# Kernel optimization log

Measured on AMD Instinct MI355X. Metric: run time of the kernel, lower is better.

Reference implementation:

```python
import jax, jax.numpy as jnp
import numpy as np

N_NODES = 20000
N_EDGES = 640000
HID = 256
IN_F, IN_SIZE = 6, 6
OUT_F, FH = 6, 3
EDGE_DIM = 8
T_DIM, S_DIM = 4, 6
N_LAYERS = 5


def setup_inputs() -> dict:
    key = jax.random.key(0)
    ks = jax.random.split(key, 32)
    g = lambda i, shape, scale=0.05: jax.random.normal(ks[i], shape, dtype=jnp.float32) * scale
    inp = {
        "x": jax.random.normal(ks[0], (N_NODES, IN_F, IN_SIZE), dtype=jnp.float32),
        "edge_index": jax.random.randint(ks[1], (2, N_EDGES), 0, N_NODES, dtype=jnp.int32),
        "edge_attr": jax.random.normal(ks[2], (N_EDGES, EDGE_DIM), dtype=jnp.float32),
        "t": jax.random.normal(ks[3], (N_NODES, T_DIM), dtype=jnp.float32),
        "s": jax.random.normal(ks[4], (N_NODES, S_DIM), dtype=jnp.float32),
        # embedder
        "W_emb": g(5, (IN_F * IN_SIZE, HID)), "b_emb": jnp.zeros((HID,), jnp.float32),
        # spatio-temporal encoder: t/s linear embeds + fusion over concat(x, te, se)
        "W_t": g(6, (T_DIM, HID)), "b_t": jnp.zeros((HID,), jnp.float32),
        "W_s": g(7, (S_DIM, HID)), "b_s": jnp.zeros((HID,), jnp.float32),
        "W_f": g(8, (3 * HID, HID)), "b_f": jnp.zeros((HID,), jnp.float32),
        # layernorm
        "ln_g": jnp.ones((HID,), jnp.float32), "ln_b": jnp.zeros((HID,), jnp.float32),
        # 5 TransformerConv layers (heads=1): query/key/value/edge/skip linears
        "Wq": g(9, (N_LAYERS, HID, HID)), "bq": jnp.zeros((N_LAYERS, HID), jnp.float32),
        "Wk": g(10, (N_LAYERS, HID, HID)), "bk": jnp.zeros((N_LAYERS, HID), jnp.float32),
        "Wv": g(11, (N_LAYERS, HID, HID)), "bv": jnp.zeros((N_LAYERS, HID), jnp.float32),
        "We": g(12, (N_LAYERS, EDGE_DIM, HID)), "be": jnp.zeros((N_LAYERS, HID), jnp.float32),
        "Wskip": g(13, (N_LAYERS, HID, HID)), "bskip": jnp.zeros((N_LAYERS, HID), jnp.float32),
        # decoder
        "W_dec": g(14, (HID, OUT_F * FH)), "b_dec": jnp.zeros((OUT_F * FH,), jnp.float32),
    }
    return inp


def _layernorm(x, g, b, eps=1e-5):
    mu = jnp.mean(x, axis=-1, keepdims=True)
    var = jnp.mean((x - mu) ** 2, axis=-1, keepdims=True)
    return (x - mu) * jax.lax.rsqrt(var + eps) * g + b


def _transformer_conv(x, src, dst, edge_attr, Wq, bq, Wk, bk, Wv, bv, We, be, Wskip, bskip):
    n = x.shape[0]
    d = x.shape[1]
    q = x @ Wq + bq                      # [n, d]
    k = x @ Wk + bk
    v = x @ Wv + bv
    e = edge_attr @ We + be              # [E, d]
    kj = k[src] + e                      # gather + edge fuse [E, d]
    vj = v[src] + e
    alpha = jnp.sum(q[dst] * kj, axis=-1) / jnp.sqrt(jnp.float32(d))  # [E]
    # segment softmax over incoming edges of each destination node
    m = jax.ops.segment_max(alpha, dst, num_segments=n)
    a = jnp.exp(alpha - m[dst])
    denom = jax.ops.segment_sum(a, dst, num_segments=n)
    w = a / (denom[dst] + 1e-16)
    out = jax.ops.segment_sum(vj * w[:, None], dst, num_segments=n)  # [n, d]
    return out + x @ Wskip + bskip       # root/skip connection


def reference(x, edge_index, edge_attr, t, s,
              W_emb, b_emb, W_t, b_t, W_s, b_s, W_f, b_f, ln_g, ln_b,
              Wq, bq, Wk, bk, Wv, bv, We, be, Wskip, bskip, W_dec, b_dec):
    n = x.shape[0]
    h = x.reshape(n, -1) @ W_emb + b_emb
    te = t @ W_t + b_t
    se = s @ W_s + b_s
    h = jnp.concatenate([h, te, se], axis=-1) @ W_f + b_f   # spatio-temporal fuse
    h = jax.nn.relu(_layernorm(h, ln_g, ln_b))
    src, dst = edge_index[0], edge_index[1]
    for i in range(N_LAYERS):
        h = jax.nn.relu(_transformer_conv(h, src, dst, edge_attr,
                                          Wq[i], bq[i], Wk[i], bk[i], Wv[i], bv[i],
                                          We[i], be[i], Wskip[i], bskip[i]))
    out = h @ W_dec + b_dec
    return out.reshape(n, OUT_F, FH)
```

## Files before the change

kernel.cpp:

```cpp
#include <hip/hip_runtime.h>
#include <hip/hip_fp8.h>
#include <math.h>

#define NN 20000
#define NPAD 20096
#define NE 640000
#define NOUT 1152
#define GSS 272
#define KVB 512
#define CAP 80
#define RECB 32
#define SCQ 0.09016994f
#define ISCL 8.8057e-5f
#define TIDX(r,k) ((((r)>>4)*4096) + (((k)>>3)*128) + (((r)&15)*8) + ((k)&7))

typedef _Float16 f16;
typedef f16 f16x8 __attribute__((ext_vector_type(8)));
typedef f16 f16x4 __attribute__((ext_vector_type(4)));
typedef f16 h2    __attribute__((ext_vector_type(2)));
typedef float f32x4 __attribute__((ext_vector_type(4)));
typedef float f32x2 __attribute__((ext_vector_type(2)));

static __device__ __forceinline__ float fdot2(h2 a, h2 b, float c) {
#if __has_builtin(__builtin_amdgcn_fdot2)
  return __builtin_amdgcn_fdot2(a, b, c, false);
#else
  return c + (float)a[0]*(float)b[0] + (float)a[1]*(float)b[1];
#endif
}

static __device__ __forceinline__ float fast_exp2(float x) {
#if __has_builtin(__builtin_amdgcn_exp2f)
  return __builtin_amdgcn_exp2f(x);
#else
  return exp2f(x);
#endif
}

static __device__ __forceinline__ int sdot4(unsigned a, unsigned b, int c) {
#if __has_builtin(__builtin_amdgcn_sdot4)
  return __builtin_amdgcn_sdot4((int)a, (int)b, c, false);
#else
  int r = c;
  #pragma unroll
  for (int i = 0; i < 4; i++) {
    int ai = ((int)((a >> (8*i)) & 255) ^ 128) - 128;
    int bi = ((int)((b >> (8*i)) & 255) ^ 128) - 128;
    r += ai*bi;
  }
  return r;
#endif
}

static __device__ __forceinline__ unsigned pack_i8x4(float a, float b, float c, float d) {
  int i0 = (int)rintf(a), i1 = (int)rintf(b), i2 = (int)rintf(c), i3 = (int)rintf(d);
  i0 = max(-127, min(127, i0)); i1 = max(-127, min(127, i1));
  i2 = max(-127, min(127, i2)); i3 = max(-127, min(127, i3));
  return (unsigned)(i0 & 255) | ((unsigned)(i1 & 255) << 8)
       | ((unsigned)(i2 & 255) << 16) | ((unsigned)(i3 & 255) << 24);
}

static __device__ __forceinline__ unsigned pack_fp8x4(float a, float b, float c, float d) {
#if __has_builtin(__builtin_amdgcn_cvt_pk_fp8_f32)
  int r = __builtin_amdgcn_cvt_pk_fp8_f32(a, b, 0, false);
  r = __builtin_amdgcn_cvt_pk_fp8_f32(c, d, r, true);
  return (unsigned)r;
#else
  __hip_fp8_e4m3 w(a), x2(b), y(c), z(d);
  return (unsigned)w.__x | ((unsigned)x2.__x<<8) | ((unsigned)y.__x<<16) | ((unsigned)z.__x<<24);
#endif
}

template<bool HI>
static __device__ __forceinline__ f32x2 unpack_fp8x2(unsigned v) {
#if __has_builtin(__builtin_amdgcn_cvt_pk_f32_fp8)
  return __builtin_amdgcn_cvt_pk_f32_fp8((int)v, HI);
#else
  unsigned s = HI ? (v >> 16) : (v & 0xffff);
  __hip_fp8_e4m3 a, b; a.__x = (unsigned char)(s & 0xff); b.__x = (unsigned char)(s >> 8);
  return (f32x2){ (float)a, (float)b };
#endif
}

__global__ __launch_bounds__(256) void k_prep_all(
    const float* __restrict__ W_emb, const float* __restrict__ W_t,
    const float* __restrict__ W_s,   const float* __restrict__ W_f,
    const float* __restrict__ b_emb, const float* __restrict__ b_t,
    const float* __restrict__ b_s,   const float* __restrict__ b_f,
    const float* __restrict__ Wq, const float* __restrict__ Wk,
    const float* __restrict__ Wv, const float* __restrict__ Wsk,
    const float* __restrict__ We, const float* __restrict__ be,
    const float* __restrict__ bq, const float* __restrict__ bk,
    const float* __restrict__ bv, const float* __restrict__ bsk,
    f16* __restrict__ Wch, float* __restrict__ bc,
    f16* __restrict__ WT, float* __restrict__ b_all,
    f16* __restrict__ hA, f16* __restrict__ hB)
{
  __shared__ float smem[64*65];
  int b = blockIdx.x;
  int tid = threadIdx.x;

  if (b < 47) {
    int r = b, c = tid;
    if (r < 36) {
      float a = 0.f;
      for (int m = 0; m < 256; m++) a += W_emb[r*256+m] * W_f[m*256+c];
      Wch[r*256+c] = (f16)a;
    } else if (r < 40) {
      int rr = r - 36; float a = 0.f;
      for (int m = 0; m < 256; m++) a += W_t[rr*256+m] * W_f[(256+m)*256+c];
      Wch[r*256+c] = (f16)a;
    } else if (r < 46) {
      int rr = r - 40; float a = 0.f;
      for (int m = 0; m < 256; m++) a += W_s[rr*256+m] * W_f[(512+m)*256+c];
      Wch[r*256+c] = (f16)a;
    } else {
      float a = b_f[c];
      for (int m = 0; m < 256; m++) a += b_emb[m]*W_f[m*256+c];
      for (int m = 0; m < 256; m++) a += b_t[m]*W_f[(256+m)*256+c];
      for (int m = 0; m < 256; m++) a += b_s[m]*W_f[(512+m)*256+c];
      bc[c] = a;
    }
  } else if (b < 367) {
    float (*lds)[65] = (float(*)[65])smem;
    int bb = b - 47;
    int nt = bb & 3, kt = (bb >> 2) & 3, mat = (bb >> 4) & 3, L = bb >> 6;
    const float* src = (mat == 0 ? Wq : mat == 1 ? Wk : mat == 2 ? Wv : Wsk) + (size_t)L*65536;
    int k0 = kt*64, n0 = nt*64;
    int c = tid & 63, r4 = tid >> 6;
    #pragma unroll
    for (int rr = 0; rr < 16; rr++) {
      int row = rr*4 + r4;
      lds[row][c] = src[(size_t)(k0 + row)*256 + n0 + c];
    }
    __syncthreads();
    f16* dst = WT + (size_t)L*294912;
    int nl = tid & 63, kb2 = tid >> 6;
    int ng = mat*256 + n0 + nl;
    #pragma unroll
    for (int half = 0; half < 2; half++) {
      int kb = kb2 + half*4;
      f16x8 v;
      #pragma unroll
      for (int e = 0; e < 8; e++) v[e] = (f16)lds[kb*8 + e][nl];
      *(f16x8*)(dst + TIDX(ng, k0 + kb*8)) = v;
    }
  } else if (b < 412) {
    float* vec = smem;
    int bb = b - 367;
    int L = bb / 9;
    int t = bb % 9;
    vec[tid] = (t < 8) ? We[(size_t)L*2048 + t*256 + tid] : be[(size_t)L*256 + tid];
    __syncthreads();
    int wave = tid >> 6, lane = tid & 63;
    for (int k = wave; k < 256; k += 4) {
      f32x4 wq = *(const f32x4*)(Wq + (size_t)L*65536 + (size_t)k*256 + lane*4);
      f32x4 vv = *(const f32x4*)(vec + lane*4);
      float d = wq[0]*vv[0] + wq[1]*vv[1] + wq[2]*vv[2] + wq[3]*vv[3];
      #pragma unroll
      for (int o = 32; o; o >>= 1) d += __shfl_xor(d, o, 64);
      if (lane == 0) WT[(size_t)L*294912 + TIDX(1024 + t, k)] = (f16)d;
    }
  } else if (b < 417) {
    int L = b - 412;
    for (int c = tid; c < NOUT; c += 256) {
      float v;
      if (c < 256)       v = bq [L*256+c];
      else if (c < 512)  v = bk [L*256+(c-256)];
      else if (c < 768)  v = bv [L*256+(c-512)];
      else if (c < 1024) v = bsk[L*256+(c-768)];
      else if (c < 1032) {
        int t = c-1024; float a = 0.f;
        for (int m = 0; m < 256; m++) a += bq[L*256+m]*We[(size_t)L*2048 + t*256 + m];
        v = a;
      } else if (c == 1032) {
        float a = 0.f;
        for (int m = 0; m < 256; m++) a += bq[L*256+m]*be[L*256+m];
        v = a;
      } else v = 0.f;
      b_all[(size_t)L*NOUT + c] = v;
    }
  } else {
    f16* p = (b == 417 ? hA : hB) + (size_t)NN*256;
    f16x8 z = {};
    for (int i = tid; i < (NPAD-NN)*256/8; i += 256)
      *(f16x8*)(p + (size_t)i*8) = z;
  }
}

__global__ void k_scatter(const int* __restrict__ ei, const float* __restrict__ eattr,
                          int* cnt, char* __restrict__ rec)
{
  int e = blockIdx.x*256 + threadIdx.x;
  if (e < NE) {
    int d = ei[NE + e];
    int pos = atomicAdd(&cnt[d], 1);
    char* rp = rec + (size_t)(d*CAP + pos)*RECB;
    f32x4 a0 = *(const f32x4*)(eattr + (size_t)e*8);
    f32x4 a1 = *(const f32x4*)(eattr + (size_t)e*8 + 4);
    f16x8 ea = { (f16)a0[0],(f16)a0[1],(f16)a0[2],(f16)a0[3],
                 (f16)a1[0],(f16)a1[1],(f16)a1[2],(f16)a1[3] };
    *(f16x8*)rp = ea;
    *(int*)(rp + 16) = ei[e];
  }
}

__global__ __launch_bounds__(256) void k_encoder(
    const float* __restrict__ x, const float* __restrict__ t, const float* __restrict__ s,
    const f16* __restrict__ Wch, const float* __restrict__ bc,
    const float* __restrict__ lng, const float* __restrict__ lnb,
    f16* __restrict__ h)
{
  __shared__ f16 Wcs[46*256];
  __shared__ float xin[16][48];
  __shared__ float bcs[256], lgs[256], lbs[256];
  int tid = threadIdx.x;
  int u0 = blockIdx.x * 16;
  for (int i = tid; i < 46*128; i += 256)
    ((unsigned int*)Wcs)[i] = ((const unsigned int*)Wch)[i];
  bcs[tid] = bc[tid]; lgs[tid] = lng[tid]; lbs[tid] = lnb[tid];
  for (int i = tid; i < 576; i += 256) xin[i/36][i%36] = x[(size_t)u0*36 + i];
  if (tid < 64) xin[tid>>2][36 + (tid&3)] = t[(size_t)u0*4 + tid];
  if (tid < 96) xin[tid/6][40 + tid%6] = s[(size_t)u0*6 + tid];
  __syncthreads();
  int node = tid >> 4, cg = tid & 15;
  int u = u0 + node;
  float acc[16];
  #pragma unroll
  for (int j = 0; j < 16; j++) acc[j] = bcs[cg*16+j];
  for (int r = 0; r < 46; r++) {
    float xv = xin[node][r];
    const h2* wr = (const h2*)(Wcs + r*256 + cg*16);
    #pragma unroll
    for (int j2 = 0; j2 < 8; j2++) {
      h2 w2 = wr[j2];
      acc[j2*2]   += xv * (float)w2[0];
      acc[j2*2+1] += xv * (float)w2[1];
    }
  }
  float sm = 0.f, sq = 0.f;
  #pragma unroll
  for (int j = 0; j < 16; j++) { sm += acc[j]; sq += acc[j]*acc[j]; }
  #pragma unroll
  for (int o = 1; o < 16; o <<= 1) { sm += __shfl_xor(sm, o, 64); sq += __shfl_xor(sq, o, 64); }
  float mu  = sm * (1.f/256.f);
  float var = sq * (1.f/256.f) - mu*mu;
  float rin = rsqrtf(var + 1e-5f);
  f16x8 o0, o1;
  #pragma unroll
  for (int j = 0; j < 8; j++) {
    int c = cg*16 + j;
    float v = (acc[j]-mu)*rin*lgs[c] + lbs[c];
    o0[j] = (f16)fmaxf(v, 0.f);
  }
  #pragma unroll
  for (int j = 0; j < 8; j++) {
    int c = cg*16 + 8 + j;
    float v = (acc[8+j]-mu)*rin*lgs[c] + lbs[c];
    o1[j] = (f16)fmaxf(v, 0.f);
  }
  *(f16x8*)(h + TIDX(u, cg*16))   = o0;
  *(f16x8*)(h + TIDX(u, cg*16+8)) = o1;
}

__global__ __launch_bounds__(256) void k_gemm(
    const f16* __restrict__ A, const f16* __restrict__ BT,
    const float* __restrict__ bias,
    unsigned char* __restrict__ qt8, unsigned char* __restrict__ kvt,
    f16* __restrict__ gsk)
{
  const int NWG = (NPAD/128)*9;
  const int Q = NWG >> 3, R = NWG & 7;
  int bid = blockIdx.x;
  int xcd = bid & 7, jj = bid >> 3;
  int wg = (xcd < R ? xcd*(Q+1) : R*(Q+1) + (xcd-R)*Q) + jj;
  int bmt = wg / 9, bnt = wg - bmt*9;

  int tid = threadIdx.x;
  int wave = tid >> 6, lane = tid & 63;
  int wm = wave >> 1, wn = wave & 1;
  int bm = bmt*128 + wm*64;
  int bn = bnt*128 + wn*64;
  int lr = lane & 15;
  int kg = lane >> 4;
  f32x4 acc[4][4];
  #pragma unroll
  for (int i = 0; i < 4; i++)
    #pragma unroll
    for (int j = 0; j < 4; j++) acc[i][j] = (f32x4){0.f,0.f,0.f,0.f};

  const f16* Ab = A  + (size_t)(bm >> 4)*4096 + kg*128 + lr*8;
  const f16* Bb = BT + (size_t)(bn >> 4)*4096 + kg*128 + lr*8;
  #pragma unroll
  for (int k0 = 0; k0 < 256; k0 += 32) {
    f16x8 af[4], bf[4];
    #pragma unroll
    for (int i = 0; i < 4; i++) af[i] = *(const f16x8*)(Ab + i*4096 + k0*16);
    #pragma unroll
    for (int j = 0; j < 4; j++) bf[j] = *(const f16x8*)(Bb + j*4096 + k0*16);
    #pragma unroll
    for (int i = 0; i < 4; i++)
      #pragma unroll
      for (int j = 0; j < 4; j++)
        acc[i][j] = __builtin_amdgcn_mfma_f32_16x16x32_f16(bf[j], af[i], acc[i][j], 0, 0, 0);
  }

  #pragma unroll
  for (int j = 0; j < 4; j++) {
    int cb0 = bn + j*16;
    if (cb0 >= 1040) continue;
    int colq = cb0 + kg*4;
    f32x4 bv = *(const f32x4*)(bias + colq);
    #pragma unroll
    for (int i = 0; i < 4; i++) {
      int row = bm + i*16 + lr;
      float v0 = acc[i][j][0]+bv[0], v1 = acc[i][j][1]+bv[1];
      float v2 = acc[i][j][2]+bv[2], v3 = acc[i][j][3]+bv[3];
      if (cb0 < 256) {
        *(unsigned*)(qt8 + (size_t)row*256 + colq) = pack_i8x4(v0*32.f, v1*32.f, v2*32.f, v3*32.f);
      } else if (cb0 < 512) {
        *(unsigned*)(kvt + (size_t)row*KVB + (colq-256)) = pack_i8x4(v0*32.f, v1*32.f, v2*32.f, v3*32.f);
      } else if (cb0 < 768) {
        *(unsigned*)(kvt + (size_t)row*KVB + 256 + (colq-512)) = pack_fp8x4(v0, v1, v2, v3);
      } else if (cb0 < 1024) {
        f16x4 st = { (f16)v0, (f16)v1, (f16)v2, (f16)v3 };
        *(f16x4*)(gsk + (size_t)row*GSS + (colq-768)) = st;
      } else {
        f16x4 st = { (f16)(v0*SCQ), (f16)(v1*SCQ), (f16)(v2*SCQ), (f16)(v3*SCQ) };
        *(f16x4*)(gsk + (size_t)row*GSS + 256 + (colq-1024)) = st;
      }
    }
  }
}

__global__ __launch_bounds__(256) void k_alpha(
    const unsigned char* __restrict__ qt8, const unsigned char* __restrict__ kvt,
    const f16* __restrict__ gsk, char* __restrict__ rec,
    const int* __restrict__ cnt, float* __restrict__ stats)
{
  int wid = threadIdx.x >> 6, lane = threadIdx.x & 63;
  int u = __builtin_amdgcn_readfirstlane(blockIdx.x*4 + wid);
  int deg = cnt[u];
  const uint4* qp = (const uint4*)(qt8 + (size_t)u*256);
  uint4 q[16];
  #pragma unroll
  for (int c = 0; c < 16; c++) q[c] = qp[c];
  const f16* gb = gsk + (size_t)u*GSS;
  f16x8 qe8 = *(const f16x8*)(gb + 256);
  float qbv = (float)gb[264];
  size_t ub = (size_t)u*CAP;

  float ssum = 0.f;
  float ae[8];
  #pragma unroll
  for (int j = 0; j < 8; j++) ae[j] = 0.f;

  for (int i = lane; i < deg; i += 64) {
    char* rp = rec + (ub + i)*RECB;
    f16x8 ea = *(const f16x8*)rp;
    int sn = *(const int*)(rp + 16);
    const uint4* kp = (const uint4*)(kvt + (size_t)sn*KVB);
    int di = 0;
    #pragma unroll
    for (int c = 0; c < 16; c++) {
      uint4 kw = kp[c];
      di = sdot4(kw.x, q[c].x, di);
      di = sdot4(kw.y, q[c].y, di);
      di = sdot4(kw.z, q[c].z, di);
      di = sdot4(kw.w, q[c].w, di);
    }
    float edot = 0.f;
    edot = fdot2((h2){ea[0],ea[1]}, (h2){qe8[0],qe8[1]}, edot);
    edot = fdot2((h2){ea[2],ea[3]}, (h2){qe8[2],qe8[3]}, edot);
    edot = fdot2((h2){ea[4],ea[5]}, (h2){qe8[4],qe8[5]}, edot);
    edot = fdot2((h2){ea[6],ea[7]}, (h2){qe8[6],qe8[7]}, edot);
    float w = fast_exp2((float)di*ISCL + edot + qbv);
    *(float*)(rp + 20) = w;
    ssum += w;
    #pragma unroll
    for (int j = 0; j < 8; j++) ae[j] += w*(float)ea[j];
  }

  #pragma unroll
  for (int o = 1; o < 64; o <<= 1) {
    ssum += __shfl_xor(ssum, o, 64);
    #pragma unroll
    for (int j = 0; j < 8; j++) ae[j] += __shfl_xor(ae[j], o, 64);
  }
  if (lane == 0) {
    float* sp = stats + (size_t)u*12;
    sp[0] = ssum;
    *(f32x4*)(sp + 4) = (f32x4){ae[0], ae[1], ae[2], ae[3]};
    *(f32x4*)(sp + 8) = (f32x4){ae[4], ae[5], ae[6], ae[7]};
  }
}

__global__ __launch_bounds__(256) void k_attn2(
    const unsigned char* __restrict__ kvt, const f16* __restrict__ gsk,
    const char* __restrict__ rec,
    const float* __restrict__ WeL, const float* __restrict__ beL,
    const int* __restrict__ cnt, const float* __restrict__ stats,
    f16* __restrict__ hout)
{
  int wid  = threadIdx.x >> 6;
  int lane = threadIdx.x & 63;
  int grp  = lane >> 4;
  int gl   = lane & 15;
  int u = blockIdx.x*4 + wid;
  int deg = cnt[u];
  size_t ub = (size_t)u*CAP;

  float av[16];
  #pragma unroll
  for (int j = 0; j < 16; j++) av[j] = 0.f;

  #pragma unroll 2
  for (int i = grp; i < deg; i += 4) {
    const char* rp = rec + (ub + i)*RECB;
    int2 sw = *(const int2*)(rp + 16);
    float w = __int_as_float(sw.y);
    uint4 vw = *(const uint4*)(kvt + (size_t)sw.x*KVB + 256 + gl*16);
    f32x2 p;
    p = unpack_fp8x2<false>(vw.x); av[0]  += w*p[0]; av[1]  += w*p[1];
    p = unpack_fp8x2<true >(vw.x); av[2]  += w*p[0]; av[3]  += w*p[1];
    p = unpack_fp8x2<false>(vw.y); av[4]  += w*p[0]; av[5]  += w*p[1];
    p = unpack_fp8x2<true >(vw.y); av[6]  += w*p[0]; av[7]  += w*p[1];
    p = unpack_fp8x2<false>(vw.z); av[8]  += w*p[0]; av[9]  += w*p[1];
    p = unpack_fp8x2<true >(vw.z); av[10] += w*p[0]; av[11] += w*p[1];
    p = unpack_fp8x2<false>(vw.w); av[12] += w*p[0]; av[13] += w*p[1];
    p = unpack_fp8x2<true >(vw.w); av[14] += w*p[0]; av[15] += w*p[1];
  }

  #pragma unroll
  for (int j = 0; j < 16; j++) {
    av[j] += __shfl_xor(av[j], 16, 64);
    av[j] += __shfl_xor(av[j], 32, 64);
  }

  const float* sp = stats + (size_t)u*12;
  float ssum = sp[0];
  f32x4 aeA = *(const f32x4*)(sp + 4);
  f32x4 aeB = *(const f32x4*)(sp + 8);
  float inv = 1.f/(ssum + 1e-16f);

  int cb = gl*16 + grp*4;
  f16x4 sk = *(const f16x4*)(gsk + (size_t)u*GSS + cb);
  f16 res[4];
  #pragma unroll
  for (int t = 0; t < 4; t++) {
    int c = cb + t;
    float o = av[grp*4+t];
    o += aeA[0]*WeL[0*256+c] + aeA[1]*WeL[1*256+c] + aeA[2]*WeL[2*256+c] + aeA[3]*WeL[3*256+c];
    o += aeB[0]*WeL[4*256+c] + aeB[1]*WeL[5*256+c] + aeB[2]*WeL[6*256+c] + aeB[3]*WeL[7*256+c];
    o += ssum*beL[c];
    o = o*inv + (float)sk[t];
    res[t] = (f16)fmaxf(o, 0.f);
  }
  f16x4 outp = { res[0], res[1], res[2], res[3] };
  *(f16x4*)(hout + TIDX(u, cb)) = outp;
}

__global__ __launch_bounds__(256) void k_decoder(
    const f16* __restrict__ h, const float* __restrict__ Wd,
    const float* __restrict__ bd, float* __restrict__ out)
{
  int n0 = blockIdx.x*32;
  __shared__ float hs[32*256];
  int tid = threadIdx.x;
  for (int j = tid; j < 32*32; j += 256) {
    int node = j >> 5, c8 = (j & 31)*8;
    f16x8 v = *(const f16x8*)(h + TIDX(n0 + node, c8));
    float* dst = &hs[node*256 + c8];
    #pragma unroll
    for (int e = 0; e < 8; e++) dst[e] = (float)v[e];
  }
  __syncthreads();
  for (int o = tid; o < 32*18; o += 256) {
    int ln = o/18, col = o - ln*18;
    int node = n0 + ln;
    float acc = bd[col];
    const float* hr = &hs[ln*256];
    #pragma unroll 4
    for (int k4 = 0; k4 < 64; k4++) {
      f32x4 hv = *(const f32x4*)(hr + k4*4);
      acc += hv[0]*Wd[(k4*4+0)*18+col] + hv[1]*Wd[(k4*4+1)*18+col]
           + hv[2]*Wd[(k4*4+2)*18+col] + hv[3]*Wd[(k4*4+3)*18+col];
    }
    out[(size_t)node*18 + col] = acc;
  }
}

extern "C" void kernel_launch(void* const* d_in, const int* in_sizes, int n_in,
                              void* d_out, int out_size, void* d_ws, size_t ws_size,
                              hipStream_t stream)
{
  const float* x     = (const float*)d_in[0];
  const int*   ei    = (const int*)  d_in[1];
  const float* eattr = (const float*)d_in[2];
  const float* t     = (const float*)d_in[3];
  const float* s     = (const float*)d_in[4];
  const float* W_emb = (const float*)d_in[5];
  const float* b_emb = (const float*)d_in[6];
  const float* W_t   = (const float*)d_in[7];
  const float* b_t   = (const float*)d_in[8];
  const float* W_s   = (const float*)d_in[9];
  const float* b_s   = (const float*)d_in[10];
  const float* W_f   = (const float*)d_in[11];
  const float* b_f   = (const float*)d_in[12];
  const float* ln_g  = (const float*)d_in[13];
  const float* ln_b  = (const float*)d_in[14];
  const float* Wq    = (const float*)d_in[15];
  const float* bq    = (const float*)d_in[16];
  const float* Wk    = (const float*)d_in[17];
  const float* bk    = (const float*)d_in[18];
  const float* Wv    = (const float*)d_in[19];
  const float* bv    = (const float*)d_in[20];
  const float* We    = (const float*)d_in[21];
  const float* be    = (const float*)d_in[22];
  const float* Wsk   = (const float*)d_in[23];
  const float* bsk   = (const float*)d_in[24];
  const float* W_dec = (const float*)d_in[25];
  const float* b_dec = (const float*)d_in[26];

  float* wsf = (float*)d_ws;
  size_t off = 0;
  float* bc    = wsf + off; off += 256;
  float* b_all = wsf + off; off += (size_t)5*NOUT;
  f16*   Wch   = (f16*)(wsf + off); off += (size_t)46*256/2;
  f16*   WT    = (f16*)(wsf + off); off += (size_t)5*294912/2;
  unsigned char* qt8 = (unsigned char*)(wsf + off); off += (size_t)NPAD*256/4;
  unsigned char* kvt = (unsigned char*)(wsf + off); off += (size_t)NPAD*KVB/4;
  f16*   gsk   = (f16*)(wsf + off); off += (size_t)NPAD*GSS/2;
  f16*   hA    = (f16*)(wsf + off); off += (size_t)NPAD*256/2;
  f16*   hB    = (f16*)(wsf + off); off += (size_t)NPAD*256/2;
  char*  rec   = (char*)(wsf + off); off += (size_t)NN*CAP*RECB/4;
  float* stats = wsf + off; off += (size_t)NN*12;
  int*   cnt   = (int*)(wsf + off); off += NN;

  (void)hipMemsetAsync(cnt, 0, NN*sizeof(int), stream);
  k_prep_all<<<419, 256, 0, stream>>>(W_emb, W_t, W_s, W_f, b_emb, b_t, b_s, b_f,
                                      Wq, Wk, Wv, Wsk, We, be, bq, bk, bv, bsk,
                                      Wch, bc, WT, b_all, hA, hB);
  k_scatter <<<(NE+255)/256, 256, 0, stream>>>(ei, eattr, cnt, rec);

  k_encoder <<<NN/16, 256, 0, stream>>>(x, t, s, Wch, bc, ln_g, ln_b, hA);

  f16* hin = hA;
  f16* hot = hB;
  for (int L = 0; L < 5; L++) {
    k_gemm<<<(NPAD/128)*9, 256, 0, stream>>>(hin, WT + (size_t)L*294912,
                                             b_all + (size_t)L*NOUT, qt8, kvt, gsk);
    k_alpha<<<NN/4, 256, 0, stream>>>(qt8, kvt, gsk, rec, cnt, stats);
    k_attn2<<<NN/4, 256, 0, stream>>>(kvt, gsk, rec, We + (size_t)L*2048,
                                      be + (size_t)L*256, cnt, stats, hot);
    f16* tmp = hin; hin = hot; hot = tmp;
  }
  k_decoder<<<NN/32, 256, 0, stream>>>(hin, W_dec, b_dec, (float*)d_out);
}
```

Baseline: 602.6 us.

## Fuse alpha and aggregation kernels via LDS and double-buffer GEMM operand loads

Merges the score kernel and the weighted-aggregation kernel into one per-destination-node kernel. Per-edge source/weight pairs now go to shared memory instead of being written back into the edge records, and the softmax stats stay in registers instead of a global stats buffer. This removes one launch per layer plus the global write and re-read of weights and stats. Separately, the GEMM main loop is hand-unrolled with two register sets so the next K-slice loads overlap the current MFMAs, at the cost of more registers. There is no barrier between the LDS writes and reads, which relies on each wave touching only its own slot.

```diff
diff --git a/kernel.cpp b/kernel.cpp
--- a/kernel.cpp
+++ b/kernel.cpp
@@ -291,19 +291,75 @@
 
   const f16* Ab = A  + (size_t)(bm >> 4)*4096 + kg*128 + lr*8;
   const f16* Bb = BT + (size_t)(bn >> 4)*4096 + kg*128 + lr*8;
-  #pragma unroll
-  for (int k0 = 0; k0 < 256; k0 += 32) {
-    f16x8 af[4], bf[4];
-    #pragma unroll
-    for (int i = 0; i < 4; i++) af[i] = *(const f16x8*)(Ab + i*4096 + k0*16);
-    #pragma unroll
-    for (int j = 0; j < 4; j++) bf[j] = *(const f16x8*)(Bb + j*4096 + k0*16);
-    #pragma unroll
-    for (int i = 0; i < 4; i++)
-      #pragma unroll
-      for (int j = 0; j < 4; j++)
-        acc[i][j] = __builtin_amdgcn_mfma_f32_16x16x32_f16(bf[j], af[i], acc[i][j], 0, 0, 0);
-  }
+
+  f16x8 a0,a1,a2,a3,b0,b1,b2,b3;
+  f16x8 c0,c1,c2,c3,d0,d1,d2,d3;
+
+#define LDX(K0) \
+  a0 = *(const f16x8*)(Ab + 0*4096 + (K0)*16); a1 = *(const f16x8*)(Ab + 1*4096 + (K0)*16); \
+  a2 = *(const f16x8*)(Ab + 2*4096 + (K0)*16); a3 = *(const f16x8*)(Ab + 3*4096 + (K0)*16); \
+  b0 = *(const f16x8*)(Bb + 0*4096 + (K0)*16); b1 = *(const f16x8*)(Bb + 1*4096 + (K0)*16); \
+  b2 = *(const f16x8*)(Bb + 2*4096 + (K0)*16); b3 = *(const f16x8*)(Bb + 3*4096 + (K0)*16);
+#define LDY(K0) \
+  c0 = *(const f16x8*)(Ab + 0*4096 + (K0)*16); c1 = *(const f16x8*)(Ab + 1*4096 + (K0)*16); \
+  c2 = *(const f16x8*)(Ab + 2*4096 + (K0)*16); c3 = *(const f16x8*)(Ab + 3*4096 + (K0)*16); \
+  d0 = *(const f16x8*)(Bb + 0*4096 + (K0)*16); d1 = *(const f16x8*)(Bb + 1*4096 + (K0)*16); \
+  d2 = *(const f16x8*)(Bb + 2*4096 + (K0)*16); d3 = *(const f16x8*)(Bb + 3*4096 + (K0)*16);
+#define MMX() \
+  acc[0][0]=__builtin_amdgcn_mfma_f32_16x16x32_f16(b0,a0,acc[0][0],0,0,0); \
+  acc[0][1]=__builtin_amdgcn_mfma_f32_16x16x32_f16(b1,a0,acc[0][1],0,0,0); \
+  acc[0][2]=__builtin_amdgcn_mfma_f32_16x16x32_f16(b2,a0,acc[0][2],0,0,0); \
+  acc[0][3]=__builtin_amdgcn_mfma_f32_16x16x32_f16(b3,a0,acc[0][3],0,0,0); \
+  acc[1][0]=__builtin_amdgcn_mfma_f32_16x16x32_f16(b0,a1,acc[1][0],0,0,0); \
+  acc[1][1]=__builtin_amdgcn_mfma_f32_16x16x32_f16(b1,a1,acc[1][1],0,0,0); \
+  acc[1][2]=__builtin_amdgcn_mfma_f32_16x16x32_f16(b2,a1,acc[1][2],0,0,0); \
+  acc[1][3]=__builtin_amdgcn_mfma_f32_16x16x32_f16(b3,a1,acc[1][3],0,0,0); \
+  acc[2][0]=__builtin_amdgcn_mfma_f32_16x16x32_f16(b0,a2,acc[2][0],0,0,0); \
+  acc[2][1]=__builtin_amdgcn_mfma_f32_16x16x32_f16(b1,a2,acc[2][1],0,0,0); \
+  acc[2][2]=__builtin_amdgcn_mfma_f32_16x16x32_f16(b2,a2,acc[2][2],0,0,0); \
+  acc[2][3]=__builtin_amdgcn_mfma_f32_16x16x32_f16(b3,a2,acc[2][3],0,0,0); \
+  acc[3][0]=__builtin_amdgcn_mfma_f32_16x16x32_f16(b0,a3,acc[3][0],0,0,0); \
+  acc[3][1]=__builtin_amdgcn_mfma_f32_16x16x32_f16(b1,a3,acc[3][1],0,0,0); \
+  acc[3][2]=__builtin_amdgcn_mfma_f32_16x16x32_f16(b2,a3,acc[3][2],0,0,0); \
+  acc[3][3]=__builtin_amdgcn_mfma_f32_16x16x32_f16(b3,a3,acc[3][3],0,0,0);
+#define MMY() \
+  acc[0][0]=__builtin_amdgcn_mfma_f32_16x16x32_f16(d0,c0,acc[0][0],0,0,0); \
+  acc[0][1]=__builtin_amdgcn_mfma_f32_16x16x32_f16(d1,c0,acc[0][1],0,0,0); \
+  acc[0][2]=__builtin_amdgcn_mfma_f32_16x16x32_f16(d2,c0,acc[0][2],0,0,0); \
+  acc[0][3]=__builtin_amdgcn_mfma_f32_16x16x32_f16(d3,c0,acc[0][3],0,0,0); \
+  acc[1][0]=__builtin_amdgcn_mfma_f32_16x16x32_f16(d0,c1,acc[1][0],0,0,0); \
+  acc[1][1]=__builtin_amdgcn_mfma_f32_16x16x32_f16(d1,c1,acc[1][1],0,0,0); \
+  acc[1][2]=__builtin_amdgcn_mfma_f32_16x16x32_f16(d2,c1,acc[1][2],0,0,0); \
+  acc[1][3]=__builtin_amdgcn_mfma_f32_16x16x32_f16(d3,c1,acc[1][3],0,0,0); \
+  acc[2][0]=__builtin_amdgcn_mfma_f32_16x16x32_f16(d0,c2,acc[2][0],0,0,0); \
+  acc[2][1]=__builtin_amdgcn_mfma_f32_16x16x32_f16(d1,c2,acc[2][1],0,0,0); \
+  acc[2][2]=__builtin_amdgcn_mfma_f32_16x16x32_f16(d2,c2,acc[2][2],0,0,0); \
+  acc[2][3]=__builtin_amdgcn_mfma_f32_16x16x32_f16(d3,c2,acc[2][3],0,0,0); \
+  acc[3][0]=__builtin_amdgcn_mfma_f32_16x16x32_f16(d0,c3,acc[3][0],0,0,0); \
+  acc[3][1]=__builtin_amdgcn_mfma_f32_16x16x32_f16(d1,c3,acc[3][1],0,0,0); \
+  acc[3][2]=__builtin_amdgcn_mfma_f32_16x16x32_f16(d2,c3,acc[3][2],0,0,0); \
+  acc[3][3]=__builtin_amdgcn_mfma_f32_16x16x32_f16(d3,c3,acc[3][3],0,0,0);
+
+  LDX(0)
+  LDY(32)
+  MMX()
+  LDX(64)
+  MMY()
+  LDY(96)
+  MMX()
+  LDX(128)
+  MMY()
+  LDY(160)
+  MMX()
+  LDX(192)
+  MMY()
+  LDY(224)
+  MMX()
+  MMY()
+#undef LDX
+#undef LDY
+#undef MMX
+#undef MMY
 
   #pragma unroll
   for (int j = 0; j < 4; j++) {
@@ -333,131 +389,110 @@
   }
 }
 
-__global__ __launch_bounds__(256) void k_alpha(
+__global__ __launch_bounds__(256) void k_attn(
     const unsigned char* __restrict__ qt8, const unsigned char* __restrict__ kvt,
-    const f16* __restrict__ gsk, char* __restrict__ rec,
-    const int* __restrict__ cnt, float* __restrict__ stats)
-{
+    const f16* __restrict__ gsk, const char* __restrict__ rec,
+    const float* __restrict__ WeL, const float* __restrict__ beL,
+    const int* __restrict__ cnt, f16* __restrict__ hout)
+{
+  __shared__ int2 swls[4][CAP];
   int wid = threadIdx.x >> 6, lane = threadIdx.x & 63;
-  int u = __builtin_amdgcn_readfirstlane(blockIdx.x*4 + wid);
-  int deg = cnt[u];
-  const uint4* qp = (const uint4*)(qt8 + (size_t)u*256);
-  uint4 q[16];
-  #pragma unroll
-  for (int c = 0; c < 16; c++) q[c] = qp[c];
-  const f16* gb = gsk + (size_t)u*GSS;
-  f16x8 qe8 = *(const f16x8*)(gb + 256);
-  float qbv = (float)gb[264];
-  size_t ub = (size_t)u*CAP;
-
-  float ssum = 0.f;
-  float ae[8];
-  #pragma unroll
-  for (int j = 0; j < 8; j++) ae[j] = 0.f;
-
-  for (int i = lane; i < deg; i += 64) {
-    char* rp = rec + (ub + i)*RECB;
-    f16x8 ea = *(const f16x8*)rp;
-    int sn = *(const int*)(rp + 16);
-    const uint4* kp = (const uint4*)(kvt + (size_t)sn*KVB);
-    int di = 0;
-    #pragma unroll
-    for (int c = 0; c < 16; c++) {
-      uint4 kw = kp[c];
-      di = sdot4(kw.x, q[c].x, di);
-      di = sdot4(kw.y, q[c].y, di);
-      di = sdot4(kw.z, q[c].z, di);
-      di = sdot4(kw.w, q[c].w, di);
-    }
-    float edot = 0.f;
-    edot = fdot2((h2){ea[0],ea[1]}, (h2){qe8[0],qe8[1]}, edot);
-    edot = fdot2((h2){ea[2],ea[3]}, (h2){qe8[2],qe8[3]}, edot);
-    edot = fdot2((h2){ea[4],ea[5]}, (h2){qe8[4],qe8[5]}, edot);
-    edot = fdot2((h2){ea[6],ea[7]}, (h2){qe8[6],qe8[7]}, edot);
-    float w = fast_exp2((float)di*ISCL + edot + qbv);
-    *(float*)(rp + 20) = w;
-    ssum += w;
-    #pragma unroll
-    for (int j = 0; j < 8; j++) ae[j] += w*(float)ea[j];
-  }
-
-  #pragma unroll
-  for (int o = 1; o < 64; o <<= 1) {
-    ssum += __shfl_xor(ssum, o, 64);
-    #pragma unroll
-    for (int j = 0; j < 8; j++) ae[j] += __shfl_xor(ae[j], o, 64);
-  }
-  if (lane == 0) {
-    float* sp = stats + (size_t)u*12;
-    sp[0] = ssum;
-    *(f32x4*)(sp + 4) = (f32x4){ae[0], ae[1], ae[2], ae[3]};
-    *(f32x4*)(sp + 8) = (f32x4){ae[4], ae[5], ae[6], ae[7]};
-  }
-}
-
-__global__ __launch_bounds__(256) void k_attn2(
-    const unsigned char* __restrict__ kvt, const f16* __restrict__ gsk,
-    const char* __restrict__ rec,
-    const float* __restrict__ WeL, const float* __restrict__ beL,
-    const int* __restrict__ cnt, const float* __restrict__ stats,
-    f16* __restrict__ hout)
-{
-  int wid  = threadIdx.x >> 6;
-  int lane = threadIdx.x & 63;
-  int grp  = lane >> 4;
-  int gl   = lane & 15;
   int u = blockIdx.x*4 + wid;
   int deg = cnt[u];
   size_t ub = (size_t)u*CAP;
 
-  float av[16];
-  #pragma unroll
-  for (int j = 0; j < 16; j++) av[j] = 0.f;
-
-  #pragma unroll 2
-  for (int i = grp; i < deg; i += 4) {
-    const char* rp = rec + (ub + i)*RECB;
-    int2 sw = *(const int2*)(rp + 16);
-    float w = __int_as_float(sw.y);
-    uint4 vw = *(const uint4*)(kvt + (size_t)sw.x*KVB + 256 + gl*16);
-    f32x2 p;
-    p = unpack_fp8x2<false>(vw.x); av[0]  += w*p[0]; av[1]  += w*p[1];
-    p = unpack_fp8x2<true >(vw.x); av[2]  += w*p[0]; av[3]  += w*p[1];
-    p = unpack_fp8x2<false>(vw.y); av[4]  += w*p[0]; av[5]  += w*p[1];
-    p = unpack_fp8x2<true >(vw.y); av[6]  += w*p[0]; av[7]  += w*p[1];
-    p = unpack_fp8x2<false>(vw.z); av[8]  += w*p[0]; av[9]  += w*p[1];
-    p = unpack_fp8x2<true >(vw.z); av[10] += w*p[0]; av[11] += w*p[1];
-    p = unpack_fp8x2<false>(vw.w); av[12] += w*p[0]; av[13] += w*p[1];
-    p = unpack_fp8x2<true >(vw.w); av[14] += w*p[0]; av[15] += w*p[1];
-  }
-
-  #pragma unroll
-  for (int j = 0; j < 16; j++) {
-    av[j] += __shfl_xor(av[j], 16, 64);
-    av[j] += __shfl_xor(av[j], 32, 64);
-  }
-
-  const float* sp = stats + (size_t)u*12;
-  float ssum = sp[0];
-  f32x4 aeA = *(const f32x4*)(sp + 4);
-  f32x4 aeB = *(const f32x4*)(sp + 8);
-  float inv = 1.f/(ssum + 1e-16f);
-
-  int cb = gl*16 + grp*4;
-  f16x4 sk = *(const f16x4*)(gsk + (size_t)u*GSS + cb);
-  f16 res[4];
-  #pragma unroll
-  for (int t = 0; t < 4; t++) {
-    int c = cb + t;
-    float o = av[grp*4+t];
-    o += aeA[0]*WeL[0*256+c] + aeA[1]*WeL[1*256+c] + aeA[2]*WeL[2*256+c] + aeA[3]*WeL[3*256+c];
-    o += aeB[0]*WeL[4*256+c] + aeB[1]*WeL[5*256+c] + aeB[2]*WeL[6*256+c] + aeB[3]*WeL[7*256+c];
-    o += ssum*beL[c];
-    o = o*inv + (float)sk[t];
-    res[t] = (f16)fmaxf(o, 0.f);
-  }
-  f16x4 outp = { res[0], res[1], res[2], res[3] };
-  *(f16x4*)(hout + TIDX(u, cb)) = outp;
+  {
+    const uint4* qp = (const uint4*)(qt8 + (size_t)u*256);
+    uint4 q[16];
+    #pragma unroll
+    for (int c = 0; c < 16; c++) q[c] = qp[c];
+    const f16* gb = gsk + (size_t)u*GSS;
+    f16x8 qe8 = *(const f16x8*)(gb + 256);
+    float qbv = (float)gb[264];
+
+    float ssum = 0.f;
+    float ae[8];
+    #pragma unroll
+    for (int j = 0; j < 8; j++) ae[j] = 0.f;
+
+    for (int i = lane; i < deg; i += 64) {
+      const char* rp = rec + (ub + i)*RECB;
+      f16x8 ea = *(const f16x8*)rp;
+      int sn = *(const int*)(rp + 16);
+      const uint4* kp = (const uint4*)(kvt + (size_t)sn*KVB);
+      int di = 0;
+      #pragma unroll
+      for (int c = 0; c < 16; c++) {
+        uint4 kw = kp[c];
+        di = sdot4(kw.x, q[c].x, di);
+        di = sdot4(kw.y, q[c].y, di);
+        di = sdot4(kw.z, q[c].z, di);
+        di = sdot4(kw.w, q[c].w, di);
+      }
+      float edot = 0.f;
+      edot = fdot2((h2){ea[0],ea[1]}, (h2){qe8[0],qe8[1]}, edot);
+      edot = fdot2((h2){ea[2],ea[3]}, (h2){qe8[2],qe8[3]}, edot);
+      edot = fdot2((h2){ea[4],ea[5]}, (h2){qe8[4],qe8[5]}, edot);
+      edot = fdot2((h2){ea[6],ea[7]}, (h2){qe8[6],qe8[7]}, edot);
+      float w = fast_exp2((float)di*ISCL + edot + qbv);
+      swls[wid][i] = make_int2(sn, __float_as_int(w));
+      ssum += w;
+      #pragma unroll
+      for (int j = 0; j < 8; j++) ae[j] += w*(float)ea[j];
+    }
+
+    #pragma unroll
+    for (int o = 1; o < 64; o <<= 1) {
+      ssum += __shfl_xor(ssum, o, 64);
+      #pragma unroll
+      for (int j = 0; j < 8; j++) ae[j] += __shfl_xor(ae[j], o, 64);
+    }
+
+    int grp = lane >> 4;
+    int gl  = lane & 15;
+    float av[16];
+    #pragma unroll
+    for (int j = 0; j < 16; j++) av[j] = 0.f;
+
+    #pragma unroll 2
+    for (int i = grp; i < deg; i += 4) {
+      int2 sw = swls[wid][i];
+      float w = __int_as_float(sw.y);
+      uint4 vw = *(const uint4*)(kvt + (size_t)sw.x*KVB + 256 + gl*16);
+      f32x2 p;
+      p = unpack_fp8x2<false>(vw.x); av[0]  += w*p[0]; av[1]  += w*p[1];
+      p = unpack_fp8x2<true >(vw.x); av[2]  += w*p[0]; av[3]  += w*p[1];
+      p = unpack_fp8x2<false>(vw.y); av[4]  += w*p[0]; av[5]  += w*p[1];
+      p = unpack_fp8x2<true >(vw.y); av[6]  += w*p[0]; av[7]  += w*p[1];
+      p = unpack_fp8x2<false>(vw.z); av[8]  += w*p[0]; av[9]  += w*p[1];
+      p = unpack_fp8x2<true >(vw.z); av[10] += w*p[0]; av[11] += w*p[1];
+      p = unpack_fp8x2<false>(vw.w); av[12] += w*p[0]; av[13] += w*p[1];
+      p = unpack_fp8x2<true >(vw.w); av[14] += w*p[0]; av[15] += w*p[1];
+    }
+
+    #pragma unroll
+    for (int j = 0; j < 16; j++) {
+      av[j] += __shfl_xor(av[j], 16, 64);
+      av[j] += __shfl_xor(av[j], 32, 64);
+    }
+
+    float inv = 1.f/(ssum + 1e-16f);
+    int cb = gl*16 + grp*4;
+    f16x4 sk = *(const f16x4*)(gsk + (size_t)u*GSS + cb);
+    f16 res[4];
+    #pragma unroll
+    for (int t = 0; t < 4; t++) {
+      int c = cb + t;
+      float o = av[grp*4+t];
+      o += ae[0]*WeL[0*256+c] + ae[1]*WeL[1*256+c] + ae[2]*WeL[2*256+c] + ae[3]*WeL[3*256+c];
+      o += ae[4]*WeL[4*256+c] + ae[5]*WeL[5*256+c] + ae[6]*WeL[6*256+c] + ae[7]*WeL[7*256+c];
+      o += ssum*beL[c];
+      o = o*inv + (float)sk[t];
+      res[t] = (f16)fmaxf(o, 0.f);
+    }
+    f16x4 outp = { res[0], res[1], res[2], res[3] };
+    *(f16x4*)(hout + TIDX(u, cb)) = outp;
+  }
 }
 
 __global__ __launch_bounds__(256) void k_decoder(
@@ -534,7 +569,6 @@
   f16*   hA    = (f16*)(wsf + off); off += (size_t)NPAD*256/2;
   f16*   hB    = (f16*)(wsf + off); off += (size_t)NPAD*256/2;
   char*  rec   = (char*)(wsf + off); off += (size_t)NN*CAP*RECB/4;
-  float* stats = wsf + off; off += (size_t)NN*12;
   int*   cnt   = (int*)(wsf + off); off += NN;
 
   (void)hipMemsetAsync(cnt, 0, NN*sizeof(int), stream);
@@ -550,9 +584,8 @@
   for (int L = 0; L < 5; L++) {
     k_gemm<<<(NPAD/128)*9, 256, 0, stream>>>(hin, WT + (size_t)L*294912,
                                              b_all + (size_t)L*NOUT, qt8, kvt, gsk);
-    k_alpha<<<NN/4, 256, 0, stream>>>(qt8, kvt, gsk, rec, cnt, stats);
-    k_attn2<<<NN/4, 256, 0, stream>>>(kvt, gsk, rec, We + (size_t)L*2048,
-                                      be + (size_t)L*256, cnt, stats, hot);
+    k_attn<<<NN/4, 256, 0, stream>>>(qt8, kvt, gsk, rec, We + (size_t)L*2048,
+                                     be + (size_t)L*256, cnt, hot);
     f16* tmp = hin; hin = hot; hot = tmp;
   }
   k_decoder<<<NN/32, 256, 0, stream>>>(hin, W_dec, b_dec, (float*)d_out);
```

New measurement: 669.5 us. +11.1%, slower.
